# Kernel optimization log

Hardware: AMD Instinct MI355X
Metric: run time of the kernel (lower is better)

## Reference

```python
import jax, jax.numpy as jnp
import numpy as np

DIM = 256
HEAD_DIM = 32
GRID = 8
EPS_GN = 1e-6
EPS_LN = 1e-5


def groupnorm1(x, w, b):
    # GroupNorm(1, C): normalize over (C,H,W) per sample, per-channel affine.
    m = jnp.mean(x, axis=(1, 2, 3), keepdims=True)
    v = jnp.var(x, axis=(1, 2, 3), keepdims=True)
    xn = (x - m) * jax.lax.rsqrt(v + EPS_GN)
    return xn * w[None, :, None, None] + b[None, :, None, None]


def conv1x1(x, w, b=None):
    # 1x1 conv as channel matmul; w: [out, in]
    y = jnp.einsum('bchw,oc->bohw', x, w)
    if b is not None:
        y = y + b[None, :, None, None]
    return y


def setup_inputs() -> dict:
    key = jax.random.key(0)
    ks = jax.random.split(key, 8)
    C = DIM
    s = 0.02
    return {
        'x': jax.random.normal(ks[0], (4, C, 64, 64), dtype=jnp.float32),
        'norm_w': jnp.ones((C,), jnp.float32),
        'norm_b': jnp.zeros((C,), jnp.float32),
        'qkv_w': jax.random.normal(ks[1], (3 * C, C), jnp.float32) * s,
        'qkv_b': jnp.zeros((3 * C,), jnp.float32),
        'proj_w': jax.random.normal(ks[2], (C, C), jnp.float32) * s,
        'proj_b': jnp.zeros((C,), jnp.float32),
        'grid_norm_w': jnp.ones((C,), jnp.float32),
        'grid_norm_b': jnp.zeros((C,), jnp.float32),
        'pm_ln_w': jnp.ones((4 * C,), jnp.float32),
        'pm_ln_b': jnp.zeros((4 * C,), jnp.float32),
        'pm_red_w': jax.random.normal(ks[3], (C, 4 * C), jnp.float32) * s,
        'ds_norm_w': jnp.ones((C,), jnp.float32),
        'ds_norm_b': jnp.zeros((C,), jnp.float32),
        'q_w': jax.random.normal(ks[4], (C, C), jnp.float32) * s,
        'q_b': jnp.zeros((C,), jnp.float32),
        'kv_w': jax.random.normal(ks[5], (2 * C, C), jnp.float32) * s,
        'kv_b': jnp.zeros((2 * C,), jnp.float32),
    }


def reference(x, norm_w, norm_b, qkv_w, qkv_b, proj_w, proj_b,
              grid_norm_w, grid_norm_b, pm_ln_w, pm_ln_b, pm_red_w,
              ds_norm_w, ds_norm_b, q_w, q_b, kv_w, kv_b):
    B, C, H, W = x.shape
    hd = HEAD_DIM
    nh = C // hd
    gs = GRID
    gh, gw = H // gs, W // gs
    scale = hd ** -0.5

    # ---- local windowed (grid) attention ----
    qkv = conv1x1(groupnorm1(x, norm_w, norm_b), qkv_w, qkv_b)  # [B,3C,H,W]
    qkv = qkv.reshape(B, 3, nh, hd, gh, gs, gw, gs)
    qkv = qkv.transpose(1, 0, 2, 4, 6, 5, 7, 3).reshape(3, -1, gs * gs, hd)
    q, k, v = qkv[0], qkv[1], qkv[2]
    attn = jax.nn.softmax(jnp.einsum('nqd,nkd->nqk', q * scale, k), axis=-1)
    gx = jnp.einsum('nqk,nkd->nqd', attn, v)
    gx = gx.reshape(B, nh, gh, gw, gs, gs, hd)
    gx = gx.transpose(0, 1, 6, 2, 4, 3, 5).reshape(B, C, H, W)
    grid_x = groupnorm1(x + gx, grid_norm_w, grid_norm_b)

    t = grid_x.transpose(0, 2, 3, 1)  # BHWC
    m = jnp.concatenate([t[:, 0::2, 0::2], t[:, 1::2, 0::2],
                         t[:, 0::2, 1::2], t[:, 1::2, 1::2]], axis=-1)
    m = m.reshape(B, (H // 2) * (W // 2), 4 * C)
    mu = jnp.mean(m, axis=-1, keepdims=True)
    var = jnp.var(m, axis=-1, keepdims=True)
    m = (m - mu) * jax.lax.rsqrt(var + EPS_LN) * pm_ln_w + pm_ln_b
    m = m @ pm_red_w.T  # [B, HW/4, C]
    pm = m.reshape(B, H // 2, W // 2, C).transpose(0, 3, 1, 2)

    # ---- global attention (full q attends to pooled kv) ----
    ds = groupnorm1(pm, ds_norm_w, ds_norm_b)
    qg = conv1x1(grid_x, q_w, q_b).reshape(B, nh, hd, H * W).transpose(0, 1, 3, 2)
    kvg = conv1x1(ds, kv_w, kv_b).reshape(B, 2, nh, hd, (H // 2) * (W // 2))
    kvg = kvg.transpose(1, 0, 2, 4, 3)
    kg, vg = kvg[0], kvg[1]
    attn2 = jax.nn.softmax(jnp.einsum('bnqd,bnkd->bnqk', qg * scale, kg), axis=-1)
    go = jnp.einsum('bnqk,bnkd->bnqd', attn2, vg)
    go = go.transpose(0, 1, 3, 2).reshape(B, C, H, W)
    global_x = go + grid_x

    # drop=0.0 -> identity
    return conv1x1(global_x, proj_w, proj_b)
```

## Files before the change

kernel.cpp:

```cpp
#include <hip/hip_runtime.h>
#include <hip/hip_bf16.h>

#define BATCH 4
#define CDIM 256
#define HWSZ 4096
#define P2 1024
#define SCALE 0.17677669529663687f
#define LOG2E 1.4426950408889634f
#define SCL2 (SCALE * LOG2E)
#define EPS_GN 1e-6f
#define EPS_LN 1e-5f
#define MFIX 8.0f
#define MFIX2 (MFIX * LOG2E)

typedef short v8s __attribute__((ext_vector_type(8)));
typedef float v4f __attribute__((ext_vector_type(4)));

__device__ __forceinline__ unsigned short f2bf(float f) {
    __hip_bfloat16 h = __float2bfloat16(f);
    return *reinterpret_cast<unsigned short*>(&h);
}
__device__ __forceinline__ float bf2f(unsigned short u) {
    return __uint_as_float(((unsigned int)u) << 16);
}
__device__ __forceinline__ float bflo(unsigned int u) {
    return __uint_as_float(u << 16);
}
__device__ __forceinline__ float bfhi(unsigned int u) {
    return __uint_as_float(u & 0xffff0000u);
}
__device__ __forceinline__ unsigned int pack2(float lo, float hi) {
    return (unsigned int)f2bf(lo) | ((unsigned int)f2bf(hi) << 16);
}
__device__ __forceinline__ unsigned int tpack2(float lo, float hi) {
    return (__float_as_uint(lo) >> 16) | (__float_as_uint(hi) & 0xffff0000u);
}
__device__ __forceinline__ float fexp2(float x) {
#if __has_builtin(__builtin_amdgcn_exp2f)
    return __builtin_amdgcn_exp2f(x);
#else
    return exp2f(x);
#endif
}
__device__ __forceinline__ uint2 expack2(v4f s, float& sum) {
    float a = fexp2(s[0] - MFIX2);
    float b = fexp2(s[1] - MFIX2);
    float c = fexp2(s[2] - MFIX2);
    float d = fexp2(s[3] - MFIX2);
    sum += (a + b) + (c + d);
    return make_uint2(tpack2(a, b), tpack2(c, d));
}
__device__ __forceinline__ v8s u4v8(uint2 a, uint2 b) {
    union { unsigned int u[4]; v8s v; } r;
    r.u[0] = a.x; r.u[1] = a.y; r.u[2] = b.x; r.u[3] = b.y;
    return r.v;
}
__device__ __forceinline__ int vperm(int j) {
    return (j & 0x23) | ((j & 0x0C) << 1) | ((j & 0x10) >> 2);
}
__device__ __forceinline__ void async16(void* lds, const void* g) {
    __builtin_amdgcn_global_load_lds(
        (const __attribute__((address_space(1))) unsigned int*)g,
        (__attribute__((address_space(3))) unsigned int*)lds, 16, 0, 0);
}

__global__ void gn_partial4(const float* __restrict__ a, const unsigned short* __restrict__ a2bf,
                            int pb4, int nblk, float* __restrict__ part)
{
    int bb  = blockIdx.x / nblk;
    int blk = blockIdx.x % nblk;
    const float* pa = a + (size_t)bb * pb4 * 4;
    const unsigned short* pa2 = a2bf ? a2bf + (size_t)bb * pb4 * 4 : nullptr;
    int tid = threadIdx.x;
    float s = 0.f, s2 = 0.f;
    for (int i = blk * 256 + tid; i < pb4; i += nblk * 256) {
        float4 v = *(const float4*)(pa + (size_t)i * 4);
        if (pa2) {
            uint2 g = *(const uint2*)(pa2 + (size_t)i * 4);
            v.x += bflo(g.x); v.y += bfhi(g.x);
            v.z += bflo(g.y); v.w += bfhi(g.y);
        }
        s += (v.x + v.y) + (v.z + v.w);
        s2 += fmaf(v.x, v.x, fmaf(v.y, v.y, fmaf(v.z, v.z, v.w * v.w)));
    }
    __shared__ float ls[256], ls2[256];
    ls[tid] = s; ls2[tid] = s2; __syncthreads();
    for (int off = 128; off > 0; off >>= 1) {
        if (tid < off) { ls[tid] += ls[tid + off]; ls2[tid] += ls2[tid + off]; }
        __syncthreads();
    }
    if (tid == 0) {
        part[blockIdx.x * 2]     = ls[0];
        part[blockIdx.x * 2 + 1] = ls2[0];
    }
}

__global__ void gn_finalize(const float* __restrict__ part, int nblk, float inv_n,
                            float eps, float* __restrict__ stats, int nb)
{
    int b = threadIdx.x;
    if (b < nb) {
        float s = 0.f, s2 = 0.f;
        for (int i = 0; i < nblk; i++) {
            s  += part[(b * nblk + i) * 2];
            s2 += part[(b * nblk + i) * 2 + 1];
        }
        float m = s * inv_n;
        float v = s2 * inv_n - m * m;
        stats[b * 2]     = m;
        stats[b * 2 + 1] = rsqrtf(v + eps);
    }
}

__global__ void cast_weights(const float* __restrict__ w0, const float* __restrict__ w1,
                             const float* __restrict__ w2, const float* __restrict__ w3,
                             const float* __restrict__ w4, unsigned short* __restrict__ dst)
{
    int i = blockIdx.x * 256 + threadIdx.x;
    int idx = i * 4;
    const float* src; int off;
    if      (idx < 196608) { src = w0; off = 0; }
    else if (idx < 458752) { src = w1; off = 196608; }
    else if (idx < 589824) { src = w2; off = 458752; }
    else if (idx < 655360) { src = w3; off = 589824; }
    else                   { src = w4; off = 655360; }
    float4 v = *(const float4*)(src + idx - off);
    *(uint2*)(dst + idx) = make_uint2(pack2(v.x, v.y), pack2(v.z, v.w));
}

__global__ __launch_bounds__(256) void tnc(
    const float* __restrict__ A, const unsigned short* __restrict__ A2b,
    const float* __restrict__ stats, const float* __restrict__ nw,
    const float* __restrict__ nb, unsigned short* __restrict__ dst, int P)
{
    int b = blockIdx.z, c0 = blockIdx.y * 64, p0 = blockIdx.x * 64;
    __shared__ float ld[64][65];
    int t = threadIdx.x;
    {
        int ch = t >> 2, pq = (t & 3) * 16;
        size_t base = ((size_t)b * 256 + c0 + ch) * P + p0 + pq;
        float4 f0 = *(const float4*)(A + base);
        float4 f1 = *(const float4*)(A + base + 4);
        float4 f2 = *(const float4*)(A + base + 8);
        float4 f3 = *(const float4*)(A + base + 12);
        if (A2b) {
            const unsigned short* ap = A2b + base;
            uint4 q0 = *(const uint4*)(ap);
            uint4 q1 = *(const uint4*)(ap + 8);
            f0.x += bflo(q0.x); f0.y += bfhi(q0.x); f0.z += bflo(q0.y); f0.w += bfhi(q0.y);
            f1.x += bflo(q0.z); f1.y += bfhi(q0.z); f1.z += bflo(q0.w); f1.w += bfhi(q0.w);
            f2.x += bflo(q1.x); f2.y += bfhi(q1.x); f2.z += bflo(q1.y); f2.w += bfhi(q1.y);
            f3.x += bflo(q1.z); f3.y += bfhi(q1.z); f3.z += bflo(q1.w); f3.w += bfhi(q1.w);
        }
        float sw = 1.f, sb = 0.f;
        if (stats) {
            float mean = stats[b * 2], r = stats[b * 2 + 1];
            float wv = nw[c0 + ch];
            sw = r * wv; sb = nb[c0 + ch] - mean * r * wv;
        }
        ld[ch][pq + 0]  = f0.x * sw + sb; ld[ch][pq + 1]  = f0.y * sw + sb;
        ld[ch][pq + 2]  = f0.z * sw + sb; ld[ch][pq + 3]  = f0.w * sw + sb;
        ld[ch][pq + 4]  = f1.x * sw + sb; ld[ch][pq + 5]  = f1.y * sw + sb;
        ld[ch][pq + 6]  = f1.z * sw + sb; ld[ch][pq + 7]  = f1.w * sw + sb;
        ld[ch][pq + 8]  = f2.x * sw + sb; ld[ch][pq + 9]  = f2.y * sw + sb;
        ld[ch][pq + 10] = f2.z * sw + sb; ld[ch][pq + 11] = f2.w * sw + sb;
        ld[ch][pq + 12] = f3.x * sw + sb; ld[ch][pq + 13] = f3.y * sw + sb;
        ld[ch][pq + 14] = f3.z * sw + sb; ld[ch][pq + 15] = f3.w * sw + sb;
    }
    __syncthreads();
    {
        int p = t >> 2, cb = (t & 3) * 16;
        unsigned int u[8];
        #pragma unroll
        for (int j = 0; j < 8; j++)
            u[j] = pack2(ld[cb + 2 * j][p], ld[cb + 2 * j + 1][p]);
        unsigned short* dp = dst + ((size_t)b * P + p0 + p) * 256 + c0 + cb;
        *(uint4*)(dp)     = make_uint4(u[0], u[1], u[2], u[3]);
        *(uint4*)(dp + 8) = make_uint4(u[4], u[5], u[6], u[7]);
    }
}

template<int MODE>
__global__ __launch_bounds__(256) void gemm_bf16(
    const unsigned short* __restrict__ actT,
    const unsigned short* __restrict__ Wb,
    const float* __restrict__ bias,
    float* __restrict__ out,
    unsigned short* __restrict__ aux1,
    unsigned short* __restrict__ aux2,
    int K, int P, int OC, float oscale)
{
    int b  = blockIdx.z;
    int p0 = blockIdx.x * 128;
    int m0 = blockIdx.y * 64;
    int tid = threadIdx.x;
    int w = tid >> 6, lane = tid & 63;
    int lm = lane & 15, lg = lane >> 4;
    int wm = w >> 1, wp = w & 1;
    int l8 = lane >> 3, cc = lane & 7;

    __shared__ __align__(16) unsigned short Wt[64 * 64];
    __shared__ __align__(16) unsigned short At[128 * 64];

    const unsigned short* actB = actT + (size_t)b * P * K;

    v4f acc[2][4];
    #pragma unroll
    for (int i = 0; i < 2; i++)
        #pragma unroll
        for (int j = 0; j < 4; j++) acc[i][j] = (v4f){0.f, 0.f, 0.f, 0.f};

    for (int ks = 0; ks < K; ks += 64) {
        #pragma unroll
        for (int i = 0; i < 2; i++) {
            int ml = w * 16 + i * 8 + l8;
            int g = cc ^ (ml & 7);
            async16(&Wt[(w * 16 + i * 8) * 64], Wb + (size_t)(m0 + ml) * K + ks + g * 8);
        }
        #pragma unroll
        for (int i = 0; i < 4; i++) {
            int pl = w * 32 + i * 8 + l8;
            int g = cc ^ (pl & 7);
            async16(&At[(w * 32 + i * 8) * 64], actB + (size_t)(p0 + pl) * K + ks + g * 8);
        }
        __syncthreads();
        #pragma unroll
        for (int kk = 0; kk < 2; kk++) {
            v8s af[2], bfv[4];
            #pragma unroll
            for (int mt = 0; mt < 2; mt++) {
                int m = wm * 32 + mt * 16 + lm;
                int ch = (kk * 4 + lg) ^ (m & 7);
                af[mt] = *(const v8s*)&Wt[m * 64 + ch * 8];
            }
            #pragma unroll
            for (int pt = 0; pt < 4; pt++) {
                int p = wp * 64 + pt * 16 + lm;
                int ch = (kk * 4 + lg) ^ (p & 7);
                bfv[pt] = *(const v8s*)&At[p * 64 + ch * 8];
            }
            #pragma unroll
            for (int mt = 0; mt < 2; mt++)
                #pragma unroll
                for (int pt = 0; pt < 4; pt++)
                    acc[mt][pt] = __builtin_amdgcn_mfma_f32_16x16x32_bf16(
                        af[mt], bfv[pt], acc[mt][pt], 0, 0, 0);
        }
        __syncthreads();
    }

    if constexpr (MODE == 1) {
        if (m0 < 512) {
            #pragma unroll
            for (int mt = 0; mt < 2; mt++) {
                int mch = m0 + wm * 32 + mt * 16 + lg * 4;
                float4 bs = *(const float4*)(bias + mch);
                #pragma unroll
                for (int pt = 0; pt < 4; pt++) {
                    int p = p0 + wp * 64 + pt * 16 + lm;
                    unsigned int u0 = pack2(acc[mt][pt][0] + bs.x, acc[mt][pt][1] + bs.y);
                    unsigned int u1 = pack2(acc[mt][pt][2] + bs.z, acc[mt][pt][3] + bs.w);
                    *(uint2*)(aux1 + ((size_t)(b * 4096 + p) * 512 + mch)) = make_uint2(u0, u1);
                }
            }
        } else {
            #pragma unroll
            for (int mt = 0; mt < 2; mt++) {
                #pragma unroll
                for (int r = 0; r < 4; r++) {
                    int mch = m0 + wm * 32 + mt * 16 + lg * 4 + r;
                    float bsv = bias[mch];
                    unsigned short* orow = aux2 + ((size_t)b * 256 + (mch - 512)) * 4096
                                           + p0 + wp * 64;
                    #pragma unroll
                    for (int pt = 0; pt < 4; pt++)
                        orow[pt * 16 + lm] = f2bf(acc[mt][pt][r] + bsv);
                }
            }
        }
    } else if constexpr (MODE == 2) {
        #pragma unroll
        for (int mt = 0; mt < 2; mt++) {
            int ch = m0 + wm * 32 + mt * 16 + lg * 4;
            int head = ch >> 5, d = ch & 31;
            float4 bs = *(const float4*)(bias + ch);
            #pragma unroll
            for (int pt = 0; pt < 4; pt++) {
                int p = p0 + wp * 64 + pt * 16 + lm;
                unsigned int u0 = pack2((acc[mt][pt][0] + bs.x) * oscale,
                                        (acc[mt][pt][1] + bs.y) * oscale);
                unsigned int u1 = pack2((acc[mt][pt][2] + bs.z) * oscale,
                                        (acc[mt][pt][3] + bs.w) * oscale);
                *(uint2*)(aux1 + ((size_t)(b * 8 + head) * P + p) * 32 + d) = make_uint2(u0, u1);
            }
        }
    } else if constexpr (MODE == 3) {
        #pragma unroll
        for (int mt = 0; mt < 2; mt++) {
            int ch = m0 + wm * 32 + mt * 16 + lg * 4;
            if (ch < 256) {
                int head = ch >> 5, d = ch & 31;
                float4 bs = *(const float4*)(bias + ch);
                #pragma unroll
                for (int pt = 0; pt < 4; pt++) {
                    int p = p0 + wp * 64 + pt * 16 + lm;
                    unsigned int u0 = pack2(acc[mt][pt][0] + bs.x, acc[mt][pt][1] + bs.y);
                    unsigned int u1 = pack2(acc[mt][pt][2] + bs.z, acc[mt][pt][3] + bs.w);
                    *(uint2*)(aux1 + ((size_t)(b * 8 + head) * P + p) * 32 + d) = make_uint2(u0, u1);
                }
            } else {
                int v = ch - 256;
                int head = v >> 5, d0 = v & 31;
                #pragma unroll
                for (int pt = 0; pt < 4; pt++) {
                    int p = p0 + wp * 64 + pt * 16 + lm;
                    int pos = (p & ~63) | vperm(p & 63);
                    #pragma unroll
                    for (int r = 0; r < 4; r++)
                        aux2[((size_t)(b * 8 + head) * 32 + d0 + r) * P + pos] =
                            f2bf(acc[mt][pt][r] + bias[ch + r]);
                }
            }
        }
    } else {
        #pragma unroll
        for (int mt = 0; mt < 2; mt++) {
            #pragma unroll
            for (int r = 0; r < 4; r++) {
                int m = m0 + wm * 32 + mt * 16 + lg * 4 + r;
                float bs = bias ? bias[m] : 0.f;
                float* orow = out + (size_t)b * OC * P + (size_t)m * P + p0 + wp * 64;
                #pragma unroll
                for (int pt = 0; pt < 4; pt++)
                    orow[pt * 16 + lm] = acc[mt][pt][r] + bs;
            }
        }
    }
}

__global__ __launch_bounds__(256, 4) void local_attn_mfma(
    const unsigned short* __restrict__ qkp,
    const unsigned short* __restrict__ vbb,
    unsigned short* __restrict__ gxb)
{
    int win = blockIdx.x;
    int gxc = win & 7, gy = (win >> 3) & 7, h = (win >> 6) & 7, b = win >> 9;
    int w = threadIdx.x >> 6, lane = threadIdx.x & 63;
    int m = lane & 15, g = lane >> 4;

    int rowbase = (gy * 8) * 64 + gxc * 8;
    const unsigned short* qkb = qkp + (size_t)b * 4096 * 512;
    const unsigned short* vbase = vbb + (size_t)b * 256 * 4096;

    int tq = w * 16 + m;
    int pq = rowbase + (tq >> 3) * 64 + (tq & 7);
    v8s qf = *(const v8s*)(qkb + (size_t)pq * 512 + h * 32 + g * 8);

    v8s ka[4];
    #pragma unroll
    for (int kt = 0; kt < 4; kt++) {
        int tk = kt * 16 + m;
        int pk = rowbase + (tk >> 3) * 64 + (tk & 7);
        ka[kt] = *(const v8s*)(qkb + (size_t)pk * 512 + 256 + h * 32 + g * 8);
    }
    v8s vb[2][2];
    #pragma unroll
    for (int c = 0; c < 2; c++)
        #pragma unroll
        for (int dt = 0; dt < 2; dt++) {
            const unsigned short* vp = vbase + (size_t)(h * 32 + dt * 16 + m) * 4096
                              + rowbase + (4 * c + (g >> 1)) * 64 + (g & 1) * 4;
            vb[c][dt] = u4v8(*(const uint2*)vp, *(const uint2*)(vp + 128));
        }

    const v4f zf = {0.f, 0.f, 0.f, 0.f};
    v4f s[4];
    #pragma unroll
    for (int kt = 0; kt < 4; kt++)
        s[kt] = __builtin_amdgcn_mfma_f32_16x16x32_bf16(ka[kt], qf, zf, 0, 0, 0);

    float lsum = 0.f;
    uint2 u0, u1, u2, u3;
    {
        v4f sc;
        #pragma unroll
        for (int r = 0; r < 4; r++) sc[r] = s[0][r] * SCL2;
        u0 = expack2(sc, lsum);
        #pragma unroll
        for (int r = 0; r < 4; r++) sc[r] = s[1][r] * SCL2;
        u1 = expack2(sc, lsum);
        #pragma unroll
        for (int r = 0; r < 4; r++) sc[r] = s[2][r] * SCL2;
        u2 = expack2(sc, lsum);
        #pragma unroll
        for (int r = 0; r < 4; r++) sc[r] = s[3][r] * SCL2;
        u3 = expack2(sc, lsum);
    }
    lsum += __shfl_xor(lsum, 16);
    lsum += __shfl_xor(lsum, 32);
    float inv = 1.f / lsum;

    v8s pa0 = u4v8(u0, u1), pa1 = u4v8(u2, u3);
    v4f o0 = zf, o1 = zf;
    o0 = __builtin_amdgcn_mfma_f32_16x16x32_bf16(pa0, vb[0][0], o0, 0, 0, 0);
    o1 = __builtin_amdgcn_mfma_f32_16x16x32_bf16(pa0, vb[0][1], o1, 0, 0, 0);
    o0 = __builtin_amdgcn_mfma_f32_16x16x32_bf16(pa1, vb[1][0], o0, 0, 0, 0);
    o1 = __builtin_amdgcn_mfma_f32_16x16x32_bf16(pa1, vb[1][1], o1, 0, 0, 0);

    float invq[4];
    #pragma unroll
    for (int r = 0; r < 4; r++) invq[r] = __shfl(inv, g * 4 + r);

    int t0 = w * 16 + g * 4;
    int px0 = rowbase + (t0 >> 3) * 64 + (t0 & 7);
    unsigned short* op0 = gxb + ((size_t)b * 256 + h * 32 + m) * 4096 + px0;
    *(uint2*)op0 = make_uint2(pack2(o0[0] * invq[0], o0[1] * invq[1]),
                              pack2(o0[2] * invq[2], o0[3] * invq[3]));
    unsigned short* op1 = gxb + ((size_t)b * 256 + h * 32 + 16 + m) * 4096 + px0;
    *(uint2*)op1 = make_uint2(pack2(o1[0] * invq[0], o1[1] * invq[1]),
                              pack2(o1[2] * invq[2], o1[3] * invq[3]));
}

__global__ __launch_bounds__(256) void patch_merge_ln2(
    const unsigned short* __restrict__ gxT,
    const float* __restrict__ lnw, const float* __restrict__ lnb,
    unsigned short* __restrict__ mn)
{
    int pix = blockIdx.x;
    int b = pix >> 10, op = pix & 1023;
    int oh = op >> 5, ow = op & 31;
    int t = threadIdx.x;
    const unsigned short* base = gxT + (size_t)b * 4096 * 256;
    float v[4];
    #pragma unroll
    for (int i = 0; i < 4; i++) {
        int h = 2 * oh + (i & 1);
        int w = 2 * ow + (i >> 1);
        v[i] = bf2f(base[(size_t)(h * 64 + w) * 256 + t]);
    }
    float s  = v[0] + v[1] + v[2] + v[3];
    float s2 = v[0]*v[0] + v[1]*v[1] + v[2]*v[2] + v[3]*v[3];
    __shared__ float ls[256], ls2[256];
    ls[t] = s; ls2[t] = s2; __syncthreads();
    for (int off = 128; off > 0; off >>= 1) {
        if (t < off) { ls[t] += ls[t + off]; ls2[t] += ls2[t + off]; }
        __syncthreads();
    }
    float mu  = ls[0] * (1.f / 1024.f);
    float var = ls2[0] * (1.f / 1024.f) - mu * mu;
    float r = rsqrtf(var + EPS_LN);
    unsigned short* orow = mn + (size_t)pix * 1024;
    #pragma unroll
    for (int i = 0; i < 4; i++) {
        int j = i * 256 + t;
        orow[j] = f2bf((v[i] - mu) * r * lnw[j] + lnb[j]);
    }
}

__global__ __launch_bounds__(256, 2) void global_attn_mfma(
    const unsigned short* __restrict__ qT,
    const unsigned short* __restrict__ kT,
    const unsigned short* __restrict__ vT,
    const unsigned short* __restrict__ gxT,
    unsigned short* __restrict__ projT)
{
    int blk = blockIdx.x;
    int qt = blk & 15, h = (blk >> 4) & 7, b = blk >> 7;
    int bh = b * 8 + h;
    int w = threadIdx.x >> 6, lane = threadIdx.x & 63;
    int m = lane & 15, g = lane >> 4;
    int qbase = qt * 256 + w * 64;

    const unsigned short* qp = qT + ((size_t)bh * 4096 + qbase + m) * 32 + g * 8;
    v8s qf0 = *(const v8s*)(qp);
    v8s qf1 = *(const v8s*)(qp + 16 * 32);
    v8s qf2 = *(const v8s*)(qp + 32 * 32);
    v8s qf3 = *(const v8s*)(qp + 48 * 32);

    const v4f zf = {0.f, 0.f, 0.f, 0.f};
    v4f o00 = zf, o01 = zf, o10 = zf, o11 = zf;
    v4f o20 = zf, o21 = zf, o30 = zf, o31 = zf;
    float l0 = 0.f, l1 = 0.f, l2 = 0.f, l3 = 0.f;

    const unsigned short* kbase = kT + ((size_t)bh * 1024 + m) * 32 + g * 8;
    const unsigned short* vbase = vT + ((size_t)bh * 32 + m) * 1024 + g * 8;

    v8s ka0 = *(const v8s*)(kbase);
    v8s ka1 = *(const v8s*)(kbase + 16 * 32);
    v8s ka2 = *(const v8s*)(kbase + 32 * 32);
    v8s ka3 = *(const v8s*)(kbase + 48 * 32);
    v8s vb0 = *(const v8s*)(vbase);
    v8s vb1 = *(const v8s*)(vbase + 16 * 1024);
    v8s vb2 = *(const v8s*)(vbase + 32);
    v8s vb3 = *(const v8s*)(vbase + 32 + 16 * 1024);

    #pragma unroll 2
    for (int t = 0; t < 16; t++) {
        int kn = (t < 15 ? t + 1 : 15) * 64;
        const unsigned short* kp = kbase + (size_t)kn * 32;
        const unsigned short* vp = vbase + kn;
        v8s nk0 = *(const v8s*)(kp);
        v8s nk1 = *(const v8s*)(kp + 16 * 32);
        v8s nk2 = *(const v8s*)(kp + 32 * 32);
        v8s nk3 = *(const v8s*)(kp + 48 * 32);
        v8s nv0 = *(const v8s*)(vp);
        v8s nv1 = *(const v8s*)(vp + 16 * 1024);
        v8s nv2 = *(const v8s*)(vp + 32);
        v8s nv3 = *(const v8s*)(vp + 32 + 16 * 1024);
        __builtin_amdgcn_sched_barrier(0);

        {
            v4f s0 = __builtin_amdgcn_mfma_f32_16x16x32_bf16(ka0, qf0, zf, 0, 0, 0);
            v4f s1 = __builtin_amdgcn_mfma_f32_16x16x32_bf16(ka1, qf0, zf, 0, 0, 0);
            v4f s2 = __builtin_amdgcn_mfma_f32_16x16x32_bf16(ka2, qf0, zf, 0, 0, 0);
            v4f s3 = __builtin_amdgcn_mfma_f32_16x16x32_bf16(ka3, qf0, zf, 0, 0, 0);
            uint2 a0 = expack2(s0, l0), a1 = expack2(s1, l0);
            uint2 a2 = expack2(s2, l0), a3 = expack2(s3, l0);
            v8s pa0 = u4v8(a0, a1), pa1 = u4v8(a2, a3);
            o00 = __builtin_amdgcn_mfma_f32_16x16x32_bf16(pa0, vb0, o00, 0, 0, 0);
            o01 = __builtin_amdgcn_mfma_f32_16x16x32_bf16(pa0, vb1, o01, 0, 0, 0);
            o00 = __builtin_amdgcn_mfma_f32_16x16x32_bf16(pa1, vb2, o00, 0, 0, 0);
            o01 = __builtin_amdgcn_mfma_f32_16x16x32_bf16(pa1, vb3, o01, 0, 0, 0);
        }
        {
            v4f s0 = __builtin_amdgcn_mfma_f32_16x16x32_bf16(ka0, qf1, zf, 0, 0, 0);
            v4f s1 = __builtin_amdgcn_mfma_f32_16x16x32_bf16(ka1, qf1, zf, 0, 0, 0);
            v4f s2 = __builtin_amdgcn_mfma_f32_16x16x32_bf16(ka2, qf1, zf, 0, 0, 0);
            v4f s3 = __builtin_amdgcn_mfma_f32_16x16x32_bf16(ka3, qf1, zf, 0, 0, 0);
            uint2 a0 = expack2(s0, l1), a1 = expack2(s1, l1);
            uint2 a2 = expack2(s2, l1), a3 = expack2(s3, l1);
            v8s pa0 = u4v8(a0, a1), pa1 = u4v8(a2, a3);
            o10 = __builtin_amdgcn_mfma_f32_16x16x32_bf16(pa0, vb0, o10, 0, 0, 0);
            o11 = __builtin_amdgcn_mfma_f32_16x16x32_bf16(pa0, vb1, o11, 0, 0, 0);
            o10 = __builtin_amdgcn_mfma_f32_16x16x32_bf16(pa1, vb2, o10, 0, 0, 0);
            o11 = __builtin_amdgcn_mfma_f32_16x16x32_bf16(pa1, vb3, o11, 0, 0, 0);
        }
        {
            v4f s0 = __builtin_amdgcn_mfma_f32_16x16x32_bf16(ka0, qf2, zf, 0, 0, 0);
            v4f s1 = __builtin_amdgcn_mfma_f32_16x16x32_bf16(ka1, qf2, zf, 0, 0, 0);
            v4f s2 = __builtin_amdgcn_mfma_f32_16x16x32_bf16(ka2, qf2, zf, 0, 0, 0);
            v4f s3 = __builtin_amdgcn_mfma_f32_16x16x32_bf16(ka3, qf2, zf, 0, 0, 0);
            uint2 a0 = expack2(s0, l2), a1 = expack2(s1, l2);
            uint2 a2 = expack2(s2, l2), a3 = expack2(s3, l2);
            v8s pa0 = u4v8(a0, a1), pa1 = u4v8(a2, a3);
            o20 = __builtin_amdgcn_mfma_f32_16x16x32_bf16(pa0, vb0, o20, 0, 0, 0);
            o21 = __builtin_amdgcn_mfma_f32_16x16x32_bf16(pa0, vb1, o21, 0, 0, 0);
            o20 = __builtin_amdgcn_mfma_f32_16x16x32_bf16(pa1, vb2, o20, 0, 0, 0);
            o21 = __builtin_amdgcn_mfma_f32_16x16x32_bf16(pa1, vb3, o21, 0, 0, 0);
        }
        {
            v4f s0 = __builtin_amdgcn_mfma_f32_16x16x32_bf16(ka0, qf3, zf, 0, 0, 0);
            v4f s1 = __builtin_amdgcn_mfma_f32_16x16x32_bf16(ka1, qf3, zf, 0, 0, 0);
            v4f s2 = __builtin_amdgcn_mfma_f32_16x16x32_bf16(ka2, qf3, zf, 0, 0, 0);
            v4f s3 = __builtin_amdgcn_mfma_f32_16x16x32_bf16(ka3, qf3, zf, 0, 0, 0);
            uint2 a0 = expack2(s0, l3), a1 = expack2(s1, l3);
            uint2 a2 = expack2(s2, l3), a3 = expack2(s3, l3);
            v8s pa0 = u4v8(a0, a1), pa1 = u4v8(a2, a3);
            o30 = __builtin_amdgcn_mfma_f32_16x16x32_bf16(pa0, vb0, o30, 0, 0, 0);
            o31 = __builtin_amdgcn_mfma_f32_16x16x32_bf16(pa0, vb1, o31, 0, 0, 0);
            o30 = __builtin_amdgcn_mfma_f32_16x16x32_bf16(pa1, vb2, o30, 0, 0, 0);
            o31 = __builtin_amdgcn_mfma_f32_16x16x32_bf16(pa1, vb3, o31, 0, 0, 0);
        }

        ka0 = nk0; ka1 = nk1; ka2 = nk2; ka3 = nk3;
        vb0 = nv0; vb1 = nv1; vb2 = nv2; vb3 = nv3;
    }

    float lf[4] = {l0, l1, l2, l3};
    v4f oq0[4] = {o00, o10, o20, o30};
    v4f oq1[4] = {o01, o11, o21, o31};
    #pragma unroll
    for (int qi = 0; qi < 4; qi++) {
        float lfq = lf[qi];
        lfq += __shfl_xor(lfq, 16);
        lfq += __shfl_xor(lfq, 32);
        float inv = 1.f / lfq;
        float invq[4];
        #pragma unroll
        for (int r = 0; r < 4; r++) invq[r] = __shfl(inv, g * 4 + r);
        #pragma unroll
        for (int r = 0; r < 4; r++) {
            size_t row = ((size_t)b * 4096 + qbase + qi * 16 + g * 4 + r) * 256 + h * 32;
            projT[row + m]      = f2bf(bf2f(gxT[row + m])      + oq0[qi][r] * invq[r]);
            projT[row + 16 + m] = f2bf(bf2f(gxT[row + 16 + m]) + oq1[qi][r] * invq[r]);
        }
    }
}

extern "C" void kernel_launch(void* const* d_in, const int* in_sizes, int n_in,
                              void* d_out, int out_size, void* d_ws, size_t ws_size,
                              hipStream_t stream)
{
    const float* x           = (const float*)d_in[0];
    const float* norm_w      = (const float*)d_in[1];
    const float* norm_b      = (const float*)d_in[2];
    const float* qkv_w       = (const float*)d_in[3];
    const float* qkv_b       = (const float*)d_in[4];
    const float* proj_w      = (const float*)d_in[5];
    const float* proj_b      = (const float*)d_in[6];
    const float* grid_norm_w = (const float*)d_in[7];
    const float* grid_norm_b = (const float*)d_in[8];
    const float* pm_ln_w     = (const float*)d_in[9];
    const float* pm_ln_b     = (const float*)d_in[10];
    const float* pm_red_w    = (const float*)d_in[11];
    const float* ds_norm_w   = (const float*)d_in[12];
    const float* ds_norm_b   = (const float*)d_in[13];
    const float* q_w         = (const float*)d_in[14];
    const float* q_b         = (const float*)d_in[15];
    const float* kv_w        = (const float*)d_in[16];
    const float* kv_b        = (const float*)d_in[17];
    float* out = (float*)d_out;

    float* wsf = (float*)d_ws;
    unsigned short* qkp   = (unsigned short*)(wsf);
    unsigned short* vbb   = (unsigned short*)(wsf + 4194304);
    unsigned short* mnb   = (unsigned short*)(wsf);
    unsigned short* kTu   = (unsigned short*)(wsf);
    unsigned short* vTu   = (unsigned short*)(wsf + 524288);
    float* pm             = wsf + 2097152;
    unsigned short* pmT   = (unsigned short*)(wsf + 3145728);
    unsigned short* qTu   = (unsigned short*)(wsf + 10485760);
    unsigned short* gxb   = (unsigned short*)(wsf + 12582912);
    unsigned short* projT = (unsigned short*)(wsf + 12582912);
    unsigned short* xT    = (unsigned short*)(wsf + 16777216);
    unsigned short* gxT   = (unsigned short*)(wsf + 16777216);
    float* part   = wsf + 18874368;
    float* stats0 = part + 512;
    float* stats1 = stats0 + 8;
    float* stats2 = stats1 + 8;
    unsigned short* wbf   = (unsigned short*)(wsf + 18875392);
    unsigned short* wbf_qkv  = wbf;
    unsigned short* wbf_pm   = wbf + 196608;
    unsigned short* wbf_kv   = wbf + 458752;
    unsigned short* wbf_q    = wbf + 589824;
    unsigned short* wbf_proj = wbf + 655360;

    cast_weights<<<704, 256, 0, stream>>>(qkv_w, pm_red_w, kv_w, q_w, proj_w, wbf);
    gn_partial4<<<BATCH * 64, 256, 0, stream>>>(x, nullptr, 262144, 64, part);
    gn_finalize<<<1, 64, 0, stream>>>(part, 64, 1.f / 1048576.f, EPS_GN, stats0, BATCH);
    tnc<<<dim3(64, 4, BATCH), 256, 0, stream>>>(x, nullptr, stats0, norm_w, norm_b, xT, 4096);
    gemm_bf16<1><<<dim3(32, 12, BATCH), 256, 0, stream>>>(
        xT, wbf_qkv, qkv_b, nullptr, qkp, vbb, 256, 4096, 768, 1.f);
    local_attn_mfma<<<2048, 256, 0, stream>>>(qkp, vbb, gxb);
    gn_partial4<<<BATCH * 64, 256, 0, stream>>>(x, gxb, 262144, 64, part);
    gn_finalize<<<1, 64, 0, stream>>>(part, 64, 1.f / 1048576.f, EPS_GN, stats1, BATCH);
    tnc<<<dim3(64, 4, BATCH), 256, 0, stream>>>(x, gxb, stats1, grid_norm_w, grid_norm_b, gxT, 4096);
    patch_merge_ln2<<<4096, 256, 0, stream>>>(gxT, pm_ln_w, pm_ln_b, mnb);
    gemm_bf16<0><<<dim3(8, 4, BATCH), 256, 0, stream>>>(
        mnb, wbf_pm, nullptr, pm, nullptr, nullptr, 1024, 1024, 256, 1.f);
    gn_partial4<<<BATCH * 16, 256, 0, stream>>>(pm, nullptr, 65536, 16, part);
    gn_finalize<<<1, 64, 0, stream>>>(part, 16, 1.f / 262144.f, EPS_GN, stats2, BATCH);
    tnc<<<dim3(16, 4, BATCH), 256, 0, stream>>>(pm, nullptr, stats2, ds_norm_w, ds_norm_b, pmT, 1024);
    gemm_bf16<3><<<dim3(8, 8, BATCH), 256, 0, stream>>>(
        pmT, wbf_kv, kv_b, nullptr, kTu, vTu, 256, 1024, 512, 1.f);
    gemm_bf16<2><<<dim3(32, 4, BATCH), 256, 0, stream>>>(
        gxT, wbf_q, q_b, nullptr, qTu, nullptr, 256, 4096, 256, SCL2);
    global_attn_mfma<<<512, 256, 0, stream>>>(qTu, kTu, vTu, gxT, projT);
    gemm_bf16<0><<<dim3(32, 4, BATCH), 256, 0, stream>>>(
        projT, wbf_proj, proj_b, out, nullptr, nullptr, 256, 4096, 256, 1.f);
}
```

Measured before the change: 175.9 us.

## Fold GroupNorm finalize into transpose kernel and enlarge GEMM tile to 128x128

Removes the three single-block gn_finalize launches: each tnc block now reduces the per-batch partial sums itself with wavefront shuffles before normalizing. The bf16 GEMM's output-channel tile grows from 64 to 128, so each wave computes 4x4 MFMA tiles, and all grids halve in the y dimension. This aims to cut launch overhead and serialization, and to improve weight/activation reuse per block. In exchange it uses more registers and LDS per block, and grids are smaller, so small GEMMs such as the 8x2x4 patch-merge one may underfill the GPU.

```diff
diff --git a/kernel.cpp b/kernel.cpp
--- a/kernel.cpp
+++ b/kernel.cpp
@@ -95,23 +95,6 @@
     }
 }
 
-__global__ void gn_finalize(const float* __restrict__ part, int nblk, float inv_n,
-                            float eps, float* __restrict__ stats, int nb)
-{
-    int b = threadIdx.x;
-    if (b < nb) {
-        float s = 0.f, s2 = 0.f;
-        for (int i = 0; i < nblk; i++) {
-            s  += part[(b * nblk + i) * 2];
-            s2 += part[(b * nblk + i) * 2 + 1];
-        }
-        float m = s * inv_n;
-        float v = s2 * inv_n - m * m;
-        stats[b * 2]     = m;
-        stats[b * 2 + 1] = rsqrtf(v + eps);
-    }
-}
-
 __global__ void cast_weights(const float* __restrict__ w0, const float* __restrict__ w1,
                              const float* __restrict__ w2, const float* __restrict__ w3,
                              const float* __restrict__ w4, unsigned short* __restrict__ dst)
@@ -130,12 +113,34 @@
 
 __global__ __launch_bounds__(256) void tnc(
     const float* __restrict__ A, const unsigned short* __restrict__ A2b,
-    const float* __restrict__ stats, const float* __restrict__ nw,
-    const float* __restrict__ nb, unsigned short* __restrict__ dst, int P)
+    const float* __restrict__ part, int nblk, float inv_n, float eps,
+    const float* __restrict__ nw, const float* __restrict__ nb,
+    unsigned short* __restrict__ dst, int P)
 {
     int b = blockIdx.z, c0 = blockIdx.y * 64, p0 = blockIdx.x * 64;
     __shared__ float ld[64][65];
+    __shared__ float sstat[2];
     int t = threadIdx.x;
+    if (t < 64) {
+        float s = 0.f, s2 = 0.f;
+        if (t < nblk) {
+            s  = part[(b * nblk + t) * 2];
+            s2 = part[(b * nblk + t) * 2 + 1];
+        }
+        #pragma unroll
+        for (int off = 32; off > 0; off >>= 1) {
+            s  += __shfl_down(s, off);
+            s2 += __shfl_down(s2, off);
+        }
+        if (t == 0) {
+            float mval = s * inv_n;
+            float var  = s2 * inv_n - mval * mval;
+            sstat[0] = mval;
+            sstat[1] = rsqrtf(var + eps);
+        }
+    }
+    __syncthreads();
+    float mean = sstat[0], rstd = sstat[1];
     {
         int ch = t >> 2, pq = (t & 3) * 16;
         size_t base = ((size_t)b * 256 + c0 + ch) * P + p0 + pq;
@@ -152,12 +157,9 @@
             f2.x += bflo(q1.x); f2.y += bfhi(q1.x); f2.z += bflo(q1.y); f2.w += bfhi(q1.y);
             f3.x += bflo(q1.z); f3.y += bfhi(q1.z); f3.z += bflo(q1.w); f3.w += bfhi(q1.w);
         }
-        float sw = 1.f, sb = 0.f;
-        if (stats) {
-            float mean = stats[b * 2], r = stats[b * 2 + 1];
-            float wv = nw[c0 + ch];
-            sw = r * wv; sb = nb[c0 + ch] - mean * r * wv;
-        }
+        float wv = nw[c0 + ch];
+        float sw = rstd * wv;
+        float sb = nb[c0 + ch] - mean * rstd * wv;
         ld[ch][pq + 0]  = f0.x * sw + sb; ld[ch][pq + 1]  = f0.y * sw + sb;
         ld[ch][pq + 2]  = f0.z * sw + sb; ld[ch][pq + 3]  = f0.w * sw + sb;
         ld[ch][pq + 4]  = f1.x * sw + sb; ld[ch][pq + 5]  = f1.y * sw + sb;
@@ -181,7 +183,7 @@
 }
 
 template<int MODE>
-__global__ __launch_bounds__(256) void gemm_bf16(
+__global__ __launch_bounds__(256, 3) void gemm_bf16(
     const unsigned short* __restrict__ actT,
     const unsigned short* __restrict__ Wb,
     const float* __restrict__ bias,
@@ -192,44 +194,44 @@
 {
     int b  = blockIdx.z;
     int p0 = blockIdx.x * 128;
-    int m0 = blockIdx.y * 64;
+    int m0 = blockIdx.y * 128;
     int tid = threadIdx.x;
     int w = tid >> 6, lane = tid & 63;
     int lm = lane & 15, lg = lane >> 4;
     int wm = w >> 1, wp = w & 1;
     int l8 = lane >> 3, cc = lane & 7;
 
-    __shared__ __align__(16) unsigned short Wt[64 * 64];
+    __shared__ __align__(16) unsigned short Wt[128 * 64];
     __shared__ __align__(16) unsigned short At[128 * 64];
 
     const unsigned short* actB = actT + (size_t)b * P * K;
 
-    v4f acc[2][4];
-    #pragma unroll
-    for (int i = 0; i < 2; i++)
+    v4f acc[4][4];
+    #pragma unroll
+    for (int i = 0; i < 4; i++)
         #pragma unroll
         for (int j = 0; j < 4; j++) acc[i][j] = (v4f){0.f, 0.f, 0.f, 0.f};
 
     for (int ks = 0; ks < K; ks += 64) {
         #pragma unroll
-        for (int i = 0; i < 2; i++) {
-            int ml = w * 16 + i * 8 + l8;
+        for (int i = 0; i < 4; i++) {
+            int ml = w * 32 + i * 8 + l8;
             int g = cc ^ (ml & 7);
-            async16(&Wt[(w * 16 + i * 8) * 64], Wb + (size_t)(m0 + ml) * K + ks + g * 8);
+            async16(&Wt[ml * 64], Wb + (size_t)(m0 + ml) * K + ks + g * 8);
         }
         #pragma unroll
         for (int i = 0; i < 4; i++) {
             int pl = w * 32 + i * 8 + l8;
             int g = cc ^ (pl & 7);
-            async16(&At[(w * 32 + i * 8) * 64], actB + (size_t)(p0 + pl) * K + ks + g * 8);
+            async16(&At[pl * 64], actB + (size_t)(p0 + pl) * K + ks + g * 8);
         }
         __syncthreads();
         #pragma unroll
         for (int kk = 0; kk < 2; kk++) {
-            v8s af[2], bfv[4];
+            v8s af[4], bfv[4];
             #pragma unroll
-            for (int mt = 0; mt < 2; mt++) {
-                int m = wm * 32 + mt * 16 + lm;
+            for (int mt = 0; mt < 4; mt++) {
+                int m = wm * 64 + mt * 16 + lm;
                 int ch = (kk * 4 + lg) ^ (m & 7);
                 af[mt] = *(const v8s*)&Wt[m * 64 + ch * 8];
             }
@@ -240,7 +242,7 @@
                 bfv[pt] = *(const v8s*)&At[p * 64 + ch * 8];
             }
             #pragma unroll
-            for (int mt = 0; mt < 2; mt++)
+            for (int mt = 0; mt < 4; mt++)
                 #pragma unroll
                 for (int pt = 0; pt < 4; pt++)
                     acc[mt][pt] = __builtin_amdgcn_mfma_f32_16x16x32_bf16(
@@ -252,8 +254,8 @@
     if constexpr (MODE == 1) {
         if (m0 < 512) {
             #pragma unroll
-            for (int mt = 0; mt < 2; mt++) {
-                int mch = m0 + wm * 32 + mt * 16 + lg * 4;
+            for (int mt = 0; mt < 4; mt++) {
+                int mch = m0 + wm * 64 + mt * 16 + lg * 4;
                 float4 bs = *(const float4*)(bias + mch);
                 #pragma unroll
                 for (int pt = 0; pt < 4; pt++) {
@@ -265,10 +267,10 @@
             }
         } else {
             #pragma unroll
-            for (int mt = 0; mt < 2; mt++) {
+            for (int mt = 0; mt < 4; mt++) {
                 #pragma unroll
                 for (int r = 0; r < 4; r++) {
-                    int mch = m0 + wm * 32 + mt * 16 + lg * 4 + r;
+                    int mch = m0 + wm * 64 + mt * 16 + lg * 4 + r;
                     float bsv = bias[mch];
                     unsigned short* orow = aux2 + ((size_t)b * 256 + (mch - 512)) * 4096
                                            + p0 + wp * 64;
@@ -280,8 +282,8 @@
         }
     } else if constexpr (MODE == 2) {
         #pragma unroll
-        for (int mt = 0; mt < 2; mt++) {
-            int ch = m0 + wm * 32 + mt * 16 + lg * 4;
+        for (int mt = 0; mt < 4; mt++) {
+            int ch = m0 + wm * 64 + mt * 16 + lg * 4;
             int head = ch >> 5, d = ch & 31;
             float4 bs = *(const float4*)(bias + ch);
             #pragma unroll
@@ -296,8 +298,8 @@
         }
     } else if constexpr (MODE == 3) {
         #pragma unroll
-        for (int mt = 0; mt < 2; mt++) {
-            int ch = m0 + wm * 32 + mt * 16 + lg * 4;
+        for (int mt = 0; mt < 4; mt++) {
+            int ch = m0 + wm * 64 + mt * 16 + lg * 4;
             if (ch < 256) {
                 int head = ch >> 5, d = ch & 31;
                 float4 bs = *(const float4*)(bias + ch);
@@ -324,10 +326,10 @@
         }
     } else {
         #pragma unroll
-        for (int mt = 0; mt < 2; mt++) {
+        for (int mt = 0; mt < 4; mt++) {
             #pragma unroll
             for (int r = 0; r < 4; r++) {
-                int m = m0 + wm * 32 + mt * 16 + lg * 4 + r;
+                int m = m0 + wm * 64 + mt * 16 + lg * 4 + r;
                 float bs = bias ? bias[m] : 0.f;
                 float* orow = out + (size_t)b * OC * P + (size_t)m * P + p0 + wp * 64;
                 #pragma unroll
@@ -625,9 +627,6 @@
     unsigned short* xT    = (unsigned short*)(wsf + 16777216);
     unsigned short* gxT   = (unsigned short*)(wsf + 16777216);
     float* part   = wsf + 18874368;
-    float* stats0 = part + 512;
-    float* stats1 = stats0 + 8;
-    float* stats2 = stats1 + 8;
     unsigned short* wbf   = (unsigned short*)(wsf + 18875392);
     unsigned short* wbf_qkv  = wbf;
     unsigned short* wbf_pm   = wbf + 196608;
@@ -637,25 +636,25 @@
 
     cast_weights<<<704, 256, 0, stream>>>(qkv_w, pm_red_w, kv_w, q_w, proj_w, wbf);
     gn_partial4<<<BATCH * 64, 256, 0, stream>>>(x, nullptr, 262144, 64, part);
-    gn_finalize<<<1, 64, 0, stream>>>(part, 64, 1.f / 1048576.f, EPS_GN, stats0, BATCH);
-    tnc<<<dim3(64, 4, BATCH), 256, 0, stream>>>(x, nullptr, stats0, norm_w, norm_b, xT, 4096);
-    gemm_bf16<1><<<dim3(32, 12, BATCH), 256, 0, stream>>>(
+    tnc<<<dim3(64, 4, BATCH), 256, 0, stream>>>(
+        x, nullptr, part, 64, 1.f / 1048576.f, EPS_GN, norm_w, norm_b, xT, 4096);
+    gemm_bf16<1><<<dim3(32, 6, BATCH), 256, 0, stream>>>(
         xT, wbf_qkv, qkv_b, nullptr, qkp, vbb, 256, 4096, 768, 1.f);
     local_attn_mfma<<<2048, 256, 0, stream>>>(qkp, vbb, gxb);
     gn_partial4<<<BATCH * 64, 256, 0, stream>>>(x, gxb, 262144, 64, part);
-    gn_finalize<<<1, 64, 0, stream>>>(part, 64, 1.f / 1048576.f, EPS_GN, stats1, BATCH);
-    tnc<<<dim3(64, 4, BATCH), 256, 0, stream>>>(x, gxb, stats1, grid_norm_w, grid_norm_b, gxT, 4096);
+    tnc<<<dim3(64, 4, BATCH), 256, 0, stream>>>(
+        x, gxb, part, 64, 1.f / 1048576.f, EPS_GN, grid_norm_w, grid_norm_b, gxT, 4096);
     patch_merge_ln2<<<4096, 256, 0, stream>>>(gxT, pm_ln_w, pm_ln_b, mnb);
-    gemm_bf16<0><<<dim3(8, 4, BATCH), 256, 0, stream>>>(
+    gemm_bf16<0><<<dim3(8, 2, BATCH), 256, 0, stream>>>(
         mnb, wbf_pm, nullptr, pm, nullptr, nullptr, 1024, 1024, 256, 1.f);
     gn_partial4<<<BATCH * 16, 256, 0, stream>>>(pm, nullptr, 65536, 16, part);
-    gn_finalize<<<1, 64, 0, stream>>>(part, 16, 1.f / 262144.f, EPS_GN, stats2, BATCH);
-    tnc<<<dim3(16, 4, BATCH), 256, 0, stream>>>(pm, nullptr, stats2, ds_norm_w, ds_norm_b, pmT, 1024);
-    gemm_bf16<3><<<dim3(8, 8, BATCH), 256, 0, stream>>>(
+    tnc<<<dim3(16, 4, BATCH), 256, 0, stream>>>(
+        pm, nullptr, part, 16, 1.f / 262144.f, EPS_GN, ds_norm_w, ds_norm_b, pmT, 1024);
+    gemm_bf16<3><<<dim3(8, 4, BATCH), 256, 0, stream>>>(
         pmT, wbf_kv, kv_b, nullptr, kTu, vTu, 256, 1024, 512, 1.f);
-    gemm_bf16<2><<<dim3(32, 4, BATCH), 256, 0, stream>>>(
+    gemm_bf16<2><<<dim3(32, 2, BATCH), 256, 0, stream>>>(
         gxT, wbf_q, q_b, nullptr, qTu, nullptr, 256, 4096, 256, SCL2);
     global_attn_mfma<<<512, 256, 0, stream>>>(qTu, kTu, vTu, gxT, projT);
-    gemm_bf16<0><<<dim3(32, 4, BATCH), 256, 0, stream>>>(
+    gemm_bf16<0><<<dim3(32, 2, BATCH), 256, 0, stream>>>(
         projT, wbf_proj, proj_b, out, nullptr, nullptr, 256, 4096, 256, 1.f);
 }
```

After: 167.4 us. 4.8% less time.
